# Performance work log

Measured on AMD Instinct MI355X. Metric: run time of the kernel, lower is better.

## Reference

```python
import jax, jax.numpy as jnp
import numpy as np

N = 50000          # total nodes
E = 800000         # edges (avg degree 16)
IN = 128           # in_feat
HID = 64           # hidden per head
HEADS = (4, 4, 1)
NEG_SLOPE = 0.2    # DGL GATConv leaky_relu default


def setup_inputs() -> dict:
    key = jax.random.key(0)
    ks = jax.random.split(key, 16)

    def w(k, shape, fan_in):
        return jax.random.normal(k, shape, jnp.float32) / np.float32(np.sqrt(fan_in))

    inp = {
        "feat": jax.random.normal(ks[0], (N, IN), jnp.float32),
        "src": jax.random.randint(ks[1], (E,), 0, N, jnp.int32),
        "dst": jax.random.randint(ks[2], (E,), 0, N, jnp.int32),
    }
    dims = [(IN, HEADS[0]), (HID * HEADS[0], HEADS[1]), (HID * HEADS[1], HEADS[2])]
    j = 3
    for i, (din, h) in enumerate(dims, 1):
        inp[f"W{i}"] = w(ks[j], (din, h * HID), din); j += 1
        inp[f"al{i}"] = w(ks[j], (h, HID), HID); j += 1
        inp[f"ar{i}"] = w(ks[j], (h, HID), HID); j += 1
        inp[f"b{i}"] = jnp.zeros((h * HID,), jnp.float32)
    return inp


def gat_layer(x, W, al, ar, b, src, dst, n_heads):
    # DGL GATConv: linear -> per-node attn logits -> edge leaky_relu ->
    # per-dst segment softmax -> weighted scatter-sum -> + bias
    h = (x @ W).reshape(N, n_heads, HID)                     # [N,H,D]
    el = jnp.einsum("nhd,hd->nh", h, al)                     # [N,H]
    er = jnp.einsum("nhd,hd->nh", h, ar)                     # [N,H]
    e = jax.nn.leaky_relu(el[src] + er[dst], NEG_SLOPE)      # [E,H]
    m = jax.ops.segment_max(e, dst, num_segments=N)          # [N,H]
    m = jnp.where(jnp.isfinite(m), m, 0.0)                   # empty segments -> -inf
    ex = jnp.exp(e - m[dst])                                 # [E,H]
    s = jax.ops.segment_sum(ex, dst, num_segments=N)         # [N,H]
    alpha = ex / s[dst]                                      # [E,H]
    msg = h[src] * alpha[:, :, None]                         # [E,H,D]
    out = jax.ops.segment_sum(msg, dst, num_segments=N)      # [N,H,D]
    return out + b.reshape(1, n_heads, HID)


def reference(feat, src, dst, W1, al1, ar1, b1, W2, al2, ar2, b2, W3, al3, ar3, b3):
    h = jax.nn.elu(gat_layer(feat, W1, al1, ar1, b1, src, dst, HEADS[0]))
    h = h.reshape(N, HEADS[0] * HID)                         # flatten heads
    h = jax.nn.elu(gat_layer(h, W2, al2, ar2, b2, src, dst, HEADS[1]))
    h = h.reshape(N, HEADS[1] * HID)
    h = gat_layer(h, W3, al3, ar3, b3, src, dst, HEADS[2])   # no activation
    return h.mean(axis=1)                                    # [N, HID]
```

## Files before the change

kernel.cpp:

```cpp
#include <hip/hip_runtime.h>
#include <math.h>

#define HID 64
#define NSLOPE 0.2f
#define SB 512
#define EXCAP 512

typedef __attribute__((ext_vector_type(8))) short short8v;
typedef __attribute__((ext_vector_type(4))) float float4v;

__device__ inline unsigned short f2bf(float x) {
  unsigned u = __float_as_uint(x);
  u += 0x7fffu + ((u >> 16) & 1u);
  return (unsigned short)(u >> 16);
}
__device__ inline float bf2f(unsigned short h) {
  return __uint_as_float(((unsigned)h) << 16);
}
__device__ inline float bflo(unsigned u) { return __uint_as_float(u << 16); }
__device__ inline float bfhi(unsigned u) { return __uint_as_float(u & 0xffff0000u); }

__global__ __launch_bounds__(256) void k_split(const float* __restrict__ x,
    unsigned short* __restrict__ hi, unsigned short* __restrict__ lo, int n) {
  int i = blockIdx.x * 256 + threadIdx.x;
  if (i < n) {
    float v = x[i];
    unsigned short h = f2bf(v);
    hi[i] = h;
    lo[i] = f2bf(v - bf2f(h));
  }
}

__global__ __launch_bounds__(256) void k_wsplit(const float* __restrict__ W,
    unsigned short* __restrict__ Whi, unsigned short* __restrict__ Wlo, int K, int N) {
  int i = blockIdx.x * 256 + threadIdx.x;
  if (i < N * K) {
    int n = i / K, k = i - n * K;
    float v = W[(size_t)k * N + n];
    unsigned short h = f2bf(v);
    Whi[i] = h;
    Wlo[i] = f2bf(v - bf2f(h));
  }
}

__global__ __launch_bounds__(256) void gemm_split(
    const unsigned short* __restrict__ Ahi, const unsigned short* __restrict__ Alo,
    const unsigned short* __restrict__ Bhi, const unsigned short* __restrict__ Blo,
    float* __restrict__ C, unsigned short* __restrict__ Gp, int M, int Nc, int K, int H) {
  __shared__ __align__(16) unsigned short AsHi[128 * 40];
  __shared__ __align__(16) unsigned short AsLo[128 * 40];
  __shared__ __align__(16) unsigned short BsHi[128 * 40];
  __shared__ __align__(16) unsigned short BsLo[128 * 40];
  const int tid = threadIdx.x;
  const int lane = tid & 63, wid = tid >> 6;
  const int wr = wid >> 1, wc = wid & 1;
  const int row0 = blockIdx.y * 128;
  const int col0 = blockIdx.x * 128;
  float4v acc[4][4];
  #pragma unroll
  for (int mi = 0; mi < 4; ++mi)
    #pragma unroll
    for (int ni = 0; ni < 4; ++ni)
      acc[mi][ni] = (float4v){0.f, 0.f, 0.f, 0.f};

  const int sr = tid >> 2;
  const int sc8 = (tid & 3) * 8;
  const int lr = lane & 15, lk = (lane >> 4) * 8;

  for (int k0 = 0; k0 < K; k0 += 32) {
    #pragma unroll
    for (int half = 0; half < 2; ++half) {
      int row = sr + half * 64;
      int arow = row0 + row; if (arow > M - 1) arow = M - 1;
      int brow = col0 + row; if (brow > Nc - 1) brow = Nc - 1;
      *(short8v*)&AsHi[row * 40 + sc8] = *(const short8v*)&Ahi[(size_t)arow * K + k0 + sc8];
      *(short8v*)&AsLo[row * 40 + sc8] = *(const short8v*)&Alo[(size_t)arow * K + k0 + sc8];
      *(short8v*)&BsHi[row * 40 + sc8] = *(const short8v*)&Bhi[(size_t)brow * K + k0 + sc8];
      *(short8v*)&BsLo[row * 40 + sc8] = *(const short8v*)&Blo[(size_t)brow * K + k0 + sc8];
    }
    __syncthreads();
    short8v ah[4], alv[4], bh[4], bl[4];
    #pragma unroll
    for (int mi = 0; mi < 4; ++mi) {
      int r = wr * 64 + mi * 16 + lr;
      ah[mi]  = *(const short8v*)&AsHi[r * 40 + lk];
      alv[mi] = *(const short8v*)&AsLo[r * 40 + lk];
    }
    #pragma unroll
    for (int ni = 0; ni < 4; ++ni) {
      int r = wc * 64 + ni * 16 + lr;
      bh[ni] = *(const short8v*)&BsHi[r * 40 + lk];
      bl[ni] = *(const short8v*)&BsLo[r * 40 + lk];
    }
    #pragma unroll
    for (int mi = 0; mi < 4; ++mi)
      #pragma unroll
      for (int ni = 0; ni < 4; ++ni) {
        acc[mi][ni] = __builtin_amdgcn_mfma_f32_16x16x32_bf16(ah[mi], bh[ni], acc[mi][ni], 0, 0, 0);
        acc[mi][ni] = __builtin_amdgcn_mfma_f32_16x16x32_bf16(ah[mi], bl[ni], acc[mi][ni], 0, 0, 0);
        acc[mi][ni] = __builtin_amdgcn_mfma_f32_16x16x32_bf16(alv[mi], bh[ni], acc[mi][ni], 0, 0, 0);
      }
    __syncthreads();
  }
  #pragma unroll
  for (int mi = 0; mi < 4; ++mi) {
    int rbase = row0 + wr * 64 + mi * 16 + (lane >> 4) * 4;
    #pragma unroll
    for (int ni = 0; ni < 4; ++ni) {
      int cc = col0 + wc * 64 + ni * 16 + (lane & 15);
      if (cc < Nc) {
        int gcol = (cc & 63) * H + (cc >> 6);
        #pragma unroll
        for (int q = 0; q < 4; ++q) {
          int rr = rbase + q;
          if (rr < M) {
            float v = acc[mi][ni][q];
            C[(size_t)rr * Nc + cc] = v;
            Gp[(size_t)rr * Nc + gcol] = f2bf(v);
          }
        }
      }
    }
  }
}

__global__ __launch_bounds__(256) void elr_kernel(const float* __restrict__ h,
    const float* __restrict__ al, const float* __restrict__ ar,
    float* __restrict__ el, float* __restrict__ er, int H, int N) {
  int n = blockIdx.x * 4 + (threadIdx.x >> 6);
  int lane = threadIdx.x & 63;
  if (n >= N) return;
  const float* hr = h + (size_t)n * H * HID;
  for (int hh = 0; hh < H; ++hh) {
    float v = hr[hh * HID + lane];
    float a = v * al[hh * HID + lane];
    float b = v * ar[hh * HID + lane];
    #pragma unroll
    for (int o = 32; o > 0; o >>= 1) { a += __shfl_xor(a, o); b += __shfl_xor(b, o); }
    if (lane == 0) { el[n * H + hh] = a; er[n * H + hh] = b; }
  }
}

__global__ void k_count(const int* __restrict__ dst, int* __restrict__ deg, int E) {
  int e = blockIdx.x * blockDim.x + threadIdx.x;
  if (e < E) atomicAdd(&deg[dst[e]], 1);
}
__global__ __launch_bounds__(SB) void k_blocksums(const int* __restrict__ deg,
                                                  int* __restrict__ bsums, int n) {
  __shared__ int s[SB];
  int t = threadIdx.x, i = blockIdx.x * SB + t;
  s[t] = (i < n) ? deg[i] : 0;
  __syncthreads();
  for (int o = SB >> 1; o > 0; o >>= 1) { if (t < o) s[t] += s[t + o]; __syncthreads(); }
  if (t == 0) bsums[blockIdx.x] = s[0];
}
__global__ __launch_bounds__(SB) void k_scancarry(const int* __restrict__ bsums,
                                                   int* __restrict__ carry, int nb) {
  __shared__ int s[SB];
  int t = threadIdx.x;
  int v = (t < nb) ? bsums[t] : 0;
  s[t] = v; __syncthreads();
  for (int o = 1; o < SB; o <<= 1) {
    int u = (t >= o) ? s[t - o] : 0;
    __syncthreads(); s[t] += u; __syncthreads();
  }
  if (t < nb) carry[t] = s[t] - v;
}
__global__ __launch_bounds__(SB) void k_offsets(const int* __restrict__ deg,
    const int* __restrict__ carry, int* __restrict__ offs, int n, int E) {
  __shared__ int s[SB];
  int t = threadIdx.x, i = blockIdx.x * SB + t;
  int v = (i < n) ? deg[i] : 0;
  s[t] = v; __syncthreads();
  for (int o = 1; o < SB; o <<= 1) {
    int u = (t >= o) ? s[t - o] : 0;
    __syncthreads(); s[t] += u; __syncthreads();
  }
  if (i < n) offs[i] = carry[blockIdx.x] + s[t] - v;
  if (i == n) offs[n] = E;
}
__global__ void k_fill(const int* __restrict__ src, const int* __restrict__ dst,
                       const int* __restrict__ offs, int* __restrict__ cursor,
                       int* __restrict__ esrc, int E) {
  int e = blockIdx.x * blockDim.x + threadIdx.x;
  if (e < E) {
    int d = dst[e];
    int slot = offs[d] + atomicAdd(&cursor[d], 1);
    esrc[slot] = src[e];
  }
}

template<int H, bool DO_ELU, bool SPLITOUT>
__global__ __launch_bounds__(64) void agg_kernel(const unsigned short* __restrict__ gp,
    const float* __restrict__ el, const float* __restrict__ er,
    const int* __restrict__ offs, const int* __restrict__ esrc,
    const float* __restrict__ bias,
    unsigned short* __restrict__ outHi, unsigned short* __restrict__ outLo,
    float* __restrict__ outF) {
  __shared__ __align__(16) float exs[EXCAP * H];
  const int n = blockIdx.x, lane = threadIdx.x;
  const int off = offs[n];
  const int deg = offs[n + 1] - off;
  float ern[H];
  if (H == 4) {
    float4 R = *(const float4*)&er[n * 4];
    ern[0] = R.x; ern[1] = R.y; ern[2] = R.z; ern[3] = R.w;
  } else {
    ern[0] = er[n];
  }
  float sum[H];
  #pragma unroll
  for (int h = 0; h < H; ++h) sum[h] = 0.f;
  for (int base = 0; base < deg; base += 64) {
    int i = base + lane;
    if (i < deg) {
      int s = esrc[off + i];
      if (H == 4) {
        float4 L = *(const float4*)&el[s * 4];
        float lv[4] = {L.x, L.y, L.z, L.w};
        float exv[4];
        #pragma unroll
        for (int h = 0; h < 4; ++h) {
          float e = lv[h] + ern[h];
          e = e > 0.f ? e : NSLOPE * e;
          exv[h] = __expf(fminf(e, 80.f));
          sum[h] += exv[h];
        }
        if (i < EXCAP)
          *(float4*)&exs[i * 4] = make_float4(exv[0], exv[1], exv[2], exv[3]);
      } else {
        float e = el[s] + ern[0];
        e = e > 0.f ? e : NSLOPE * e;
        float x = __expf(fminf(e, 80.f));
        sum[0] += x;
        if (i < EXCAP) exs[i] = x;
      }
    }
  }
  float inv[H];
  #pragma unroll
  for (int h = 0; h < H; ++h) {
    float v = sum[h];
    #pragma unroll
    for (int o = 32; o > 0; o >>= 1) v += __shfl_xor(v, o);
    inv[h] = v > 0.f ? 1.f / v : 0.f;
  }
  __syncthreads();
  float acc[H];
  #pragma unroll
  for (int h = 0; h < H; ++h) acc[h] = 0.f;
  const int degc = deg < EXCAP ? deg : EXCAP;
  int t = 0;
  for (; t + 4 <= degc; t += 4) {
    int s0 = esrc[off + t + 0], s1 = esrc[off + t + 1];
    int s2 = esrc[off + t + 2], s3 = esrc[off + t + 3];
    if (H == 4) {
      float4 x0 = *(const float4*)&exs[(t + 0) * 4];
      float4 x1 = *(const float4*)&exs[(t + 1) * 4];
      float4 x2 = *(const float4*)&exs[(t + 2) * 4];
      float4 x3 = *(const float4*)&exs[(t + 3) * 4];
      uint2 g0 = *(const uint2*)&gp[(size_t)s0 * 256 + lane * 4];
      uint2 g1 = *(const uint2*)&gp[(size_t)s1 * 256 + lane * 4];
      uint2 g2 = *(const uint2*)&gp[(size_t)s2 * 256 + lane * 4];
      uint2 g3 = *(const uint2*)&gp[(size_t)s3 * 256 + lane * 4];
      acc[0] = fmaf(bflo(g0.x), x0.x, acc[0]);
      acc[1] = fmaf(bfhi(g0.x), x0.y, acc[1]);
      acc[2] = fmaf(bflo(g0.y), x0.z, acc[2]);
      acc[3] = fmaf(bfhi(g0.y), x0.w, acc[3]);
      acc[0] = fmaf(bflo(g1.x), x1.x, acc[0]);
      acc[1] = fmaf(bfhi(g1.x), x1.y, acc[1]);
      acc[2] = fmaf(bflo(g1.y), x1.z, acc[2]);
      acc[3] = fmaf(bfhi(g1.y), x1.w, acc[3]);
      acc[0] = fmaf(bflo(g2.x), x2.x, acc[0]);
      acc[1] = fmaf(bfhi(g2.x), x2.y, acc[1]);
      acc[2] = fmaf(bflo(g2.y), x2.z, acc[2]);
      acc[3] = fmaf(bfhi(g2.y), x2.w, acc[3]);
      acc[0] = fmaf(bflo(g3.x), x3.x, acc[0]);
      acc[1] = fmaf(bfhi(g3.x), x3.y, acc[1]);
      acc[2] = fmaf(bflo(g3.y), x3.z, acc[2]);
      acc[3] = fmaf(bfhi(g3.y), x3.w, acc[3]);
    } else {
      float x0 = exs[t + 0], x1 = exs[t + 1], x2 = exs[t + 2], x3 = exs[t + 3];
      float g0 = bf2f(gp[(size_t)s0 * 64 + lane]);
      float g1 = bf2f(gp[(size_t)s1 * 64 + lane]);
      float g2 = bf2f(gp[(size_t)s2 * 64 + lane]);
      float g3 = bf2f(gp[(size_t)s3 * 64 + lane]);
      acc[0] = fmaf(g0, x0, acc[0]);
      acc[0] = fmaf(g1, x1, acc[0]);
      acc[0] = fmaf(g2, x2, acc[0]);
      acc[0] = fmaf(g3, x3, acc[0]);
    }
  }
  for (; t < degc; ++t) {
    int s = esrc[off + t];
    if (H == 4) {
      float4 x = *(const float4*)&exs[t * 4];
      uint2 g = *(const uint2*)&gp[(size_t)s * 256 + lane * 4];
      acc[0] = fmaf(bflo(g.x), x.x, acc[0]);
      acc[1] = fmaf(bfhi(g.x), x.y, acc[1]);
      acc[2] = fmaf(bflo(g.y), x.z, acc[2]);
      acc[3] = fmaf(bfhi(g.y), x.w, acc[3]);
    } else {
      acc[0] = fmaf(bf2f(gp[(size_t)s * 64 + lane]), exs[t], acc[0]);
    }
  }
  for (; t < deg; ++t) {
    int s = esrc[off + t];
    #pragma unroll
    for (int hh = 0; hh < H; ++hh) {
      float e = el[s * H + hh] + ern[hh];
      e = e > 0.f ? e : NSLOPE * e;
      float x = __expf(fminf(e, 80.f));
      float v = (H == 4) ? bf2f(gp[(size_t)s * 256 + lane * 4 + hh])
                         : bf2f(gp[(size_t)s * 64 + lane]);
      acc[hh] = fmaf(v, x, acc[hh]);
    }
  }
  #pragma unroll
  for (int hh = 0; hh < H; ++hh) {
    float v = fmaf(acc[hh], inv[hh], bias[hh * HID + lane]);
    if (DO_ELU) v = v > 0.f ? v : expm1f(v);
    size_t oi = (size_t)n * (H * HID) + hh * HID + lane;
    if (SPLITOUT) {
      unsigned short hb = f2bf(v);
      outHi[oi] = hb;
      outLo[oi] = f2bf(v - bf2f(hb));
    } else {
      outF[oi] = v;
    }
  }
}

extern "C" void kernel_launch(void* const* d_in, const int* in_sizes, int n_in,
                              void* d_out, int out_size, void* d_ws, size_t ws_size,
                              hipStream_t stream) {
  const float* feat = (const float*)d_in[0];
  const int* src = (const int*)d_in[1];
  const int* dst = (const int*)d_in[2];
  const float* W1 = (const float*)d_in[3];
  const float* al1 = (const float*)d_in[4];
  const float* ar1 = (const float*)d_in[5];
  const float* b1 = (const float*)d_in[6];
  const float* W2 = (const float*)d_in[7];
  const float* al2 = (const float*)d_in[8];
  const float* ar2 = (const float*)d_in[9];
  const float* b2 = (const float*)d_in[10];
  const float* W3 = (const float*)d_in[11];
  const float* al3 = (const float*)d_in[12];
  const float* ar3 = (const float*)d_in[13];
  const float* b3 = (const float*)d_in[14];
  const int N = in_sizes[0] / 128;
  const int E = in_sizes[1];

  char* w = (char*)d_ws;
  auto alloc = [&](size_t bytes) {
    void* p = (void*)w;
    w += (bytes + 255) & ~(size_t)255;
    return p;
  };
  unsigned short* pHi = (unsigned short*)alloc((size_t)N * 256 * 2);
  unsigned short* pLo = (unsigned short*)alloc((size_t)N * 256 * 2);
  float* Cbuf = (float*)alloc((size_t)N * 256 * 4);
  unsigned short* Gp = (unsigned short*)alloc((size_t)N * 256 * 2);
  float* el = (float*)alloc((size_t)N * 4 * 4);
  float* er = (float*)alloc((size_t)N * 4 * 4);
  int* deg = (int*)alloc((size_t)N * 4);
  int* cursor = (int*)alloc((size_t)N * 4);
  int* offs = (int*)alloc((size_t)(N + 1) * 4);
  int nb = (N + SB - 1) / SB;
  int* bsums = (int*)alloc((size_t)nb * 4);
  int* carry = (int*)alloc((size_t)nb * 4);
  int* esrc = (int*)alloc((size_t)E * 4);
  unsigned short* W1h = (unsigned short*)alloc((size_t)256 * 128 * 2);
  unsigned short* W1l = (unsigned short*)alloc((size_t)256 * 128 * 2);
  unsigned short* W2h = (unsigned short*)alloc((size_t)256 * 256 * 2);
  unsigned short* W2l = (unsigned short*)alloc((size_t)256 * 256 * 2);
  unsigned short* W3h = (unsigned short*)alloc((size_t)64 * 256 * 2);
  unsigned short* W3l = (unsigned short*)alloc((size_t)64 * 256 * 2);

  hipMemsetAsync(deg, 0, (size_t)N * 4, stream);
  hipMemsetAsync(cursor, 0, (size_t)N * 4, stream);
  int eb = (E + 255) / 256;
  k_count<<<eb, 256, 0, stream>>>(dst, deg, E);
  k_blocksums<<<nb, SB, 0, stream>>>(deg, bsums, N);
  k_scancarry<<<1, SB, 0, stream>>>(bsums, carry, nb);
  k_offsets<<<nb, SB, 0, stream>>>(deg, carry, offs, N, E);
  k_fill<<<eb, 256, 0, stream>>>(src, dst, offs, cursor, esrc, E);

  k_wsplit<<<(256 * 128 + 255) / 256, 256, 0, stream>>>(W1, W1h, W1l, 128, 256);
  k_wsplit<<<(256 * 256 + 255) / 256, 256, 0, stream>>>(W2, W2h, W2l, 256, 256);
  k_wsplit<<<(64 * 256 + 255) / 256, 256, 0, stream>>>(W3, W3h, W3l, 256, 64);

  k_split<<<((N * 128) + 255) / 256, 256, 0, stream>>>(feat, pHi, pLo, N * 128);

  int rg = (N + 127) / 128;
  int ng4 = (N + 3) / 4;
  gemm_split<<<dim3(2, rg), 256, 0, stream>>>(pHi, pLo, W1h, W1l, Cbuf, Gp, N, 256, 128, 4);
  elr_kernel<<<ng4, 256, 0, stream>>>(Cbuf, al1, ar1, el, er, 4, N);
  agg_kernel<4, true, true><<<N, 64, 0, stream>>>(Gp, el, er, offs, esrc, b1, pHi, pLo, nullptr);
  gemm_split<<<dim3(2, rg), 256, 0, stream>>>(pHi, pLo, W2h, W2l, Cbuf, Gp, N, 256, 256, 4);
  elr_kernel<<<ng4, 256, 0, stream>>>(Cbuf, al2, ar2, el, er, 4, N);
  agg_kernel<4, true, true><<<N, 64, 0, stream>>>(Gp, el, er, offs, esrc, b2, pHi, pLo, nullptr);
  gemm_split<<<dim3(1, rg), 256, 0, stream>>>(pHi, pLo, W3h, W3l, Cbuf, Gp, N, 64, 256, 1);
  elr_kernel<<<ng4, 256, 0, stream>>>(Cbuf, al3, ar3, el, er, 1, N);
  agg_kernel<1, false, false><<<N, 64, 0, stream>>>(Gp, el, er, offs, esrc, b3, nullptr, nullptr, (float*)d_out);
}
```

Measured before the change: 464.4 us.

## Pack four nodes per aggregation block and widen gather unroll to eight

The aggregation kernel now runs four wavefronts per 256-thread block, one destination node per wavefront, each with its own LDS slice. The block barrier becomes a wave-local LDS wait. The per-edge exp cache capacity is halved, which cuts LDS per wave and should allow more resident waves. The gather loop is unrolled to eight edges, with source indices fetched as two int4 loads, to keep more memory requests in flight. The risks are that the int4 index loads may be misaligned, and that nodes above degree 256 fall back to the slower tail path.

Result: slower. 490.2 us (+5.6%).

```diff
diff --git a/kernel.cpp b/kernel.cpp
--- a/kernel.cpp
+++ b/kernel.cpp
@@ -4,7 +4,7 @@
 #define HID 64
 #define NSLOPE 0.2f
 #define SB 512
-#define EXCAP 512
+#define EXCAP 256
 
 typedef __attribute__((ext_vector_type(8))) short short8v;
 typedef __attribute__((ext_vector_type(4))) float float4v;
@@ -191,14 +191,18 @@
 }
 
 template<int H, bool DO_ELU, bool SPLITOUT>
-__global__ __launch_bounds__(64) void agg_kernel(const unsigned short* __restrict__ gp,
+__global__ __launch_bounds__(256) void agg_kernel(const unsigned short* __restrict__ gp,
     const float* __restrict__ el, const float* __restrict__ er,
     const int* __restrict__ offs, const int* __restrict__ esrc,
     const float* __restrict__ bias,
     unsigned short* __restrict__ outHi, unsigned short* __restrict__ outLo,
-    float* __restrict__ outF) {
-  __shared__ __align__(16) float exs[EXCAP * H];
-  const int n = blockIdx.x, lane = threadIdx.x;
+    float* __restrict__ outF, int N) {
+  __shared__ __align__(16) float exs_all[4][EXCAP * H];
+  const int wv = threadIdx.x >> 6;
+  const int n = blockIdx.x * 4 + wv;
+  const int lane = threadIdx.x & 63;
+  if (n >= N) return;
+  float* exs = exs_all[wv];
   const int off = offs[n];
   const int deg = offs[n + 1] - off;
   float ern[H];
@@ -245,50 +249,36 @@
     for (int o = 32; o > 0; o >>= 1) v += __shfl_xor(v, o);
     inv[h] = v > 0.f ? 1.f / v : 0.f;
   }
-  __syncthreads();
+  asm volatile("s_waitcnt lgkmcnt(0)" ::: "memory");
   float acc[H];
   #pragma unroll
   for (int h = 0; h < H; ++h) acc[h] = 0.f;
   const int degc = deg < EXCAP ? deg : EXCAP;
   int t = 0;
-  for (; t + 4 <= degc; t += 4) {
-    int s0 = esrc[off + t + 0], s1 = esrc[off + t + 1];
-    int s2 = esrc[off + t + 2], s3 = esrc[off + t + 3];
+  for (; t + 8 <= degc; t += 8) {
+    int4 sa = *(const int4*)&esrc[off + t];
+    int4 sb = *(const int4*)&esrc[off + t + 4];
+    int s[8] = {sa.x, sa.y, sa.z, sa.w, sb.x, sb.y, sb.z, sb.w};
     if (H == 4) {
-      float4 x0 = *(const float4*)&exs[(t + 0) * 4];
-      float4 x1 = *(const float4*)&exs[(t + 1) * 4];
-      float4 x2 = *(const float4*)&exs[(t + 2) * 4];
-      float4 x3 = *(const float4*)&exs[(t + 3) * 4];
-      uint2 g0 = *(const uint2*)&gp[(size_t)s0 * 256 + lane * 4];
-      uint2 g1 = *(const uint2*)&gp[(size_t)s1 * 256 + lane * 4];
-      uint2 g2 = *(const uint2*)&gp[(size_t)s2 * 256 + lane * 4];
-      uint2 g3 = *(const uint2*)&gp[(size_t)s3 * 256 + lane * 4];
-      acc[0] = fmaf(bflo(g0.x), x0.x, acc[0]);
-      acc[1] = fmaf(bfhi(g0.x), x0.y, acc[1]);
-      acc[2] = fmaf(bflo(g0.y), x0.z, acc[2]);
-      acc[3] = fmaf(bfhi(g0.y), x0.w, acc[3]);
-      acc[0] = fmaf(bflo(g1.x), x1.x, acc[0]);
-      acc[1] = fmaf(bfhi(g1.x), x1.y, acc[1]);
-      acc[2] = fmaf(bflo(g1.y), x1.z, acc[2]);
-      acc[3] = fmaf(bfhi(g1.y), x1.w, acc[3]);
-      acc[0] = fmaf(bflo(g2.x), x2.x, acc[0]);
-      acc[1] = fmaf(bfhi(g2.x), x2.y, acc[1]);
-      acc[2] = fmaf(bflo(g2.y), x2.z, acc[2]);
-      acc[3] = fmaf(bfhi(g2.y), x2.w, acc[3]);
-      acc[0] = fmaf(bflo(g3.x), x3.x, acc[0]);
-      acc[1] = fmaf(bfhi(g3.x), x3.y, acc[1]);
-      acc[2] = fmaf(bflo(g3.y), x3.z, acc[2]);
-      acc[3] = fmaf(bfhi(g3.y), x3.w, acc[3]);
+      uint2 g[8];
+      #pragma unroll
+      for (int j = 0; j < 8; ++j)
+        g[j] = *(const uint2*)&gp[(size_t)s[j] * 256 + lane * 4];
+      #pragma unroll
+      for (int j = 0; j < 8; ++j) {
+        float4 x = *(const float4*)&exs[(t + j) * 4];
+        acc[0] = fmaf(bflo(g[j].x), x.x, acc[0]);
+        acc[1] = fmaf(bfhi(g[j].x), x.y, acc[1]);
+        acc[2] = fmaf(bflo(g[j].y), x.z, acc[2]);
+        acc[3] = fmaf(bfhi(g[j].y), x.w, acc[3]);
+      }
     } else {
-      float x0 = exs[t + 0], x1 = exs[t + 1], x2 = exs[t + 2], x3 = exs[t + 3];
-      float g0 = bf2f(gp[(size_t)s0 * 64 + lane]);
-      float g1 = bf2f(gp[(size_t)s1 * 64 + lane]);
-      float g2 = bf2f(gp[(size_t)s2 * 64 + lane]);
-      float g3 = bf2f(gp[(size_t)s3 * 64 + lane]);
-      acc[0] = fmaf(g0, x0, acc[0]);
-      acc[0] = fmaf(g1, x1, acc[0]);
-      acc[0] = fmaf(g2, x2, acc[0]);
-      acc[0] = fmaf(g3, x3, acc[0]);
+      unsigned short g[8];
+      #pragma unroll
+      for (int j = 0; j < 8; ++j) g[j] = gp[(size_t)s[j] * 64 + lane];
+      #pragma unroll
+      for (int j = 0; j < 8; ++j)
+        acc[0] = fmaf(bf2f(g[j]), exs[t + j], acc[0]);
     }
   }
   for (; t < degc; ++t) {
@@ -397,11 +387,11 @@
   int ng4 = (N + 3) / 4;
   gemm_split<<<dim3(2, rg), 256, 0, stream>>>(pHi, pLo, W1h, W1l, Cbuf, Gp, N, 256, 128, 4);
   elr_kernel<<<ng4, 256, 0, stream>>>(Cbuf, al1, ar1, el, er, 4, N);
-  agg_kernel<4, true, true><<<N, 64, 0, stream>>>(Gp, el, er, offs, esrc, b1, pHi, pLo, nullptr);
+  agg_kernel<4, true, true><<<ng4, 256, 0, stream>>>(Gp, el, er, offs, esrc, b1, pHi, pLo, nullptr, N);
   gemm_split<<<dim3(2, rg), 256, 0, stream>>>(pHi, pLo, W2h, W2l, Cbuf, Gp, N, 256, 256, 4);
   elr_kernel<<<ng4, 256, 0, stream>>>(Cbuf, al2, ar2, el, er, 4, N);
-  agg_kernel<4, true, true><<<N, 64, 0, stream>>>(Gp, el, er, offs, esrc, b2, pHi, pLo, nullptr);
+  agg_kernel<4, true, true><<<ng4, 256, 0, stream>>>(Gp, el, er, offs, esrc, b2, pHi, pLo, nullptr, N);
   gemm_split<<<dim3(1, rg), 256, 0, stream>>>(pHi, pLo, W3h, W3l, Cbuf, Gp, N, 64, 256, 1);
   elr_kernel<<<ng4, 256, 0, stream>>>(Cbuf, al3, ar3, el, er, 1, N);
-  agg_kernel<1, false, false><<<N, 64, 0, stream>>>(Gp, el, er, offs, esrc, b3, nullptr, nullptr, (float*)d_out);
-}
+  agg_kernel<1, false, false><<<ng4, 256, 0, stream>>>(Gp, el, er, offs, esrc, b3, nullptr, nullptr, (float*)d_out, N);
+}
```
